# Kernel optimization log

Measured on AMD Instinct MI355X. Metric: run time of the kernel, lower is better.

The kernel has to match this reference:

```python
import jax, jax.numpy as jnp
import numpy as np

N, E, D, ED, H = 50000, 640000, 128, 64, 128
EPS = 1e-5


def _bn(x, gamma, beta):
    # BatchNorm1d in training mode: batch stats over rows, biased variance
    mean = jnp.mean(x, axis=0)
    var = jnp.mean(jnp.square(x - mean), axis=0)
    return (x - mean) * jax.lax.rsqrt(var + EPS) * gamma + beta


def setup_inputs() -> dict:
    key = jax.random.key(0)
    ks = jax.random.split(key, 12)

    def lin(k, fan_in, fan_out):
        return jax.random.normal(k, (fan_in, fan_out), jnp.float32) / np.sqrt(fan_in)

    return {
        "h": jax.random.normal(ks[0], (N, D), jnp.float32),
        "edge_attr": jax.random.normal(ks[1], (E, ED), jnp.float32),
        # msg MLP: Linear(2D+ED->H), BN(H), ReLU, Linear(H->H)
        "W1": lin(ks[2], 2 * D + ED, H), "b1": jnp.zeros((H,), jnp.float32),
        "g1": jnp.ones((H,), jnp.float32), "be1": jnp.zeros((H,), jnp.float32),
        "W2": lin(ks[3], H, H), "b2": jnp.zeros((H,), jnp.float32),
        # upd MLP: Linear(D+H->H), BN(H), ReLU, Linear(H->D)
        "W3": lin(ks[4], D + H, H), "b3": jnp.zeros((H,), jnp.float32),
        "g2": jnp.ones((H,), jnp.float32), "be2": jnp.zeros((H,), jnp.float32),
        "W4": lin(ks[5], H, D), "b4": jnp.zeros((D,), jnp.float32),
        # residual LayerNorm
        "ln_g": jnp.ones((D,), jnp.float32), "ln_b": jnp.zeros((D,), jnp.float32),
        "edge_index": jax.random.randint(ks[6], (2, E), 0, N, jnp.int32),
        "num_nodes": N,
    }


def reference(h, edge_attr, W1, b1, g1, be1, W2, b2, W3, b3, g2, be2, W4, b4,
              ln_g, ln_b, edge_index, num_nodes):
    src, dst = edge_index[0], edge_index[1]
    # messages: MLP_msg(h_src || h_dst || e)  -> [E, H]
    msg_in = jnp.concatenate([h[src], h[dst], edge_attr], axis=-1)  # [E, 2D+ED]
    x = _bn(msg_in @ W1 + b1, g1, be1)
    messages = jax.nn.relu(x) @ W2 + b2
    # scatter-sum aggregate into dst nodes -> [N, H]
    agg = jax.ops.segment_sum(messages, dst, num_segments=num_nodes)
    # update: MLP_upd(h || agg) -> [N, D]
    u = jnp.concatenate([h, agg], axis=-1)
    y = _bn(u @ W3 + b3, g2, be2)
    h_new = jax.nn.relu(y) @ W4 + b4
    # residual + LayerNorm
    z = h + h_new
    mu = jnp.mean(z, axis=-1, keepdims=True)
    var = jnp.mean(jnp.square(z - mu), axis=-1, keepdims=True)
    return (z - mu) * jax.lax.rsqrt(var + EPS) * ln_g + ln_b
```

## Files before the change

### kernel.cpp

```cpp
#include <hip/hip_runtime.h>
#include <hip/hip_bf16.h>

#define EPS 1e-5f
#define DIMH 128
#define K1 320
#define K3 256

typedef __attribute__((ext_vector_type(8))) short bf16x8;
typedef __attribute__((ext_vector_type(4))) short bf16x4;
typedef __attribute__((ext_vector_type(4))) float f32x4;

#define MFMA(a, b, c) __builtin_amdgcn_mfma_f32_16x16x32_bf16(a, b, c, 0, 0, 0)

static __device__ __forceinline__ unsigned short f2bf(float f) {
    union { float f; unsigned u; } v; v.f = f;
    unsigned r = v.u + 0x7FFF + ((v.u >> 16) & 1);
    return (unsigned short)(r >> 16);
}
static __device__ __forceinline__ float bf2f(unsigned short u) {
    union { unsigned u; float f; } v; v.u = ((unsigned)u) << 16;
    return v.f;
}

__global__ void k_prep(const float* __restrict__ W1, const float* __restrict__ W2,
                       const float* __restrict__ W3, const float* __restrict__ W4,
                       unsigned short* __restrict__ W1t, unsigned short* __restrict__ W2t,
                       unsigned short* __restrict__ W3t, unsigned short* __restrict__ W4t) {
    int t = blockIdx.x * 256 + threadIdx.x;
    if (t < K1 * 128) { int k = t / 128, n = t % 128; W1t[n * K1 + k] = f2bf(W1[t]); }
    if (t < 128 * 128) { int k = t / 128, n = t % 128; W2t[n * 128 + k] = f2bf(W2[t]); }
    if (t < K3 * 128) { int k = t / 128, n = t % 128; W3t[n * K3 + k] = f2bf(W3[t]); }
    if (t < 128 * 128) { int k = t / 128, n = t % 128; W4t[n * 128 + k] = f2bf(W4[t]); }
}

__global__ void k_bn(const float* __restrict__ stats, const float* __restrict__ g,
                     const float* __restrict__ be, float* __restrict__ st, float cnt) {
    int c = threadIdx.x;
    float mean = stats[c] / cnt;
    float var = stats[128 + c] / cnt - mean * mean;
    float s = g[c] * rsqrtf(var + EPS);
    st[c] = s;
    st[128 + c] = be[c] - mean * s;
}

__global__ __launch_bounds__(256, 2) void k_msg1(
    const float* __restrict__ h, const float* __restrict__ ea,
    const int* __restrict__ src, const int* __restrict__ dst,
    const unsigned short* __restrict__ W1t, const float* __restrict__ b1,
    unsigned short* __restrict__ xout, float* __restrict__ stats) {
    const int LDA = K1 + 8;
    __shared__ unsigned short A[64 * (K1 + 8)];
    int tid = threadIdx.x, lane = tid & 63, w = tid >> 6;
    long e0 = (long)blockIdx.x * 64;

    bf16x8 bfr[10][2];
    {
        int n = (w << 5) + (lane & 15), kb = (lane >> 4) << 3;
#pragma unroll
        for (int nt = 0; nt < 2; ++nt) {
            const unsigned short* p = W1t + (size_t)(n + nt * 16) * K1 + kb;
#pragma unroll
            for (int ks = 0; ks < 10; ++ks) bfr[ks][nt] = *(const bf16x8*)(p + ks * 32);
        }
    }
    {
        int c16 = tid & 15, r2 = tid >> 4;
#pragma unroll
        for (int rr = 0; rr < 4; ++rr) {
            int row = rr * 16 + r2;
            long e = e0 + row;
            const float* hs = h + (size_t)src[e] * DIMH;
            const float* hd = h + (size_t)dst[e] * DIMH;
            const float* ep = ea + (size_t)e * 64;
#pragma unroll
            for (int i = 0; i < 5; ++i) {
                int col = (c16 + (i << 4)) << 2;
                float4 v;
                if (col < 128) v = *(const float4*)(hs + col);
                else if (col < 256) v = *(const float4*)(hd + col - 128);
                else v = *(const float4*)(ep + col - 256);
                union { bf16x4 v4; unsigned short s[4]; } u;
                u.s[0] = f2bf(v.x); u.s[1] = f2bf(v.y); u.s[2] = f2bf(v.z); u.s[3] = f2bf(v.w);
                *(bf16x4*)&A[row * LDA + col] = u.v4;
            }
        }
    }
    __syncthreads();

    f32x4 acc[4][2] = {};
#pragma unroll
    for (int rg = 0; rg < 4; ++rg) {
        int ab = (rg * 16 + (lane & 15)) * LDA + ((lane >> 4) << 3);
#pragma unroll
        for (int ks = 0; ks < 10; ++ks) {
            bf16x8 af = *(const bf16x8*)&A[ab + ks * 32];
            acc[rg][0] = MFMA(af, bfr[ks][0], acc[rg][0]);
            acc[rg][1] = MFMA(af, bfr[ks][1], acc[rg][1]);
        }
    }
    int c0 = (w << 5) + (lane & 15);
    float bias0 = b1[c0], bias1 = b1[c0 + 16];
    float ss[2] = {0.f, 0.f}, sq[2] = {0.f, 0.f};
#pragma unroll
    for (int rg = 0; rg < 4; ++rg)
#pragma unroll
        for (int r = 0; r < 4; ++r) {
            long row = e0 + rg * 16 + ((lane >> 4) << 2) + r;
            float v0 = acc[rg][0][r] + bias0;
            float v1 = acc[rg][1][r] + bias1;
            ss[0] += v0; sq[0] += v0 * v0;
            ss[1] += v1; sq[1] += v1 * v1;
            xout[(size_t)row * DIMH + c0] = f2bf(v0);
            xout[(size_t)row * DIMH + c0 + 16] = f2bf(v1);
        }
#pragma unroll
    for (int nt = 0; nt < 2; ++nt) {
        ss[nt] += __shfl_xor(ss[nt], 16); ss[nt] += __shfl_xor(ss[nt], 32);
        sq[nt] += __shfl_xor(sq[nt], 16); sq[nt] += __shfl_xor(sq[nt], 32);
    }
    if (lane < 16) {
        atomicAdd(&stats[c0], ss[0]);        atomicAdd(&stats[c0 + 16], ss[1]);
        atomicAdd(&stats[128 + c0], sq[0]);  atomicAdd(&stats[128 + c0 + 16], sq[1]);
    }
}

__global__ __launch_bounds__(256, 2) void k_msg2(
    const unsigned short* __restrict__ x, const int* __restrict__ dst,
    const unsigned short* __restrict__ W2t, const float* __restrict__ b2,
    const float* __restrict__ st, float* __restrict__ agg) {
    const int LDA = 136;
    __shared__ unsigned short A[64 * 136];
    __shared__ float sS[128], sT[128];
    __shared__ int dstv[64];
    int tid = threadIdx.x, lane = tid & 63, w = tid >> 6;
    long e0 = (long)blockIdx.x * 64;
    if (tid < 128) { sS[tid] = st[tid]; sT[tid] = st[128 + tid]; }
    if (tid < 64) dstv[tid] = dst[e0 + tid];

    bf16x8 bfr[4][2];
    {
        int n = (w << 5) + (lane & 15), kb = (lane >> 4) << 3;
#pragma unroll
        for (int nt = 0; nt < 2; ++nt) {
            const unsigned short* p = W2t + (size_t)(n + nt * 16) * 128 + kb;
#pragma unroll
            for (int ks = 0; ks < 4; ++ks) bfr[ks][nt] = *(const bf16x8*)(p + ks * 32);
        }
    }
    __syncthreads();
    {
        int c16 = tid & 15, r2 = tid >> 4;
#pragma unroll
        for (int rr = 0; rr < 4; ++rr) {
            int row = rr * 16 + r2;
            bf16x8 v = *(const bf16x8*)(x + (size_t)(e0 + row) * DIMH + c16 * 8);
            union { bf16x8 v8; unsigned short s[8]; } u;
#pragma unroll
            for (int j = 0; j < 8; ++j) {
                int c = c16 * 8 + j;
                float f = bf2f((unsigned short)v[j]) * sS[c] + sT[c];
                u.s[j] = f2bf(fmaxf(f, 0.f));
            }
            *(bf16x8*)&A[row * LDA + c16 * 8] = u.v8;
        }
    }
    __syncthreads();

    f32x4 acc[4][2] = {};
#pragma unroll
    for (int rg = 0; rg < 4; ++rg) {
        int ab = (rg * 16 + (lane & 15)) * LDA + ((lane >> 4) << 3);
#pragma unroll
        for (int ks = 0; ks < 4; ++ks) {
            bf16x8 af = *(const bf16x8*)&A[ab + ks * 32];
            acc[rg][0] = MFMA(af, bfr[ks][0], acc[rg][0]);
            acc[rg][1] = MFMA(af, bfr[ks][1], acc[rg][1]);
        }
    }
    int c0 = (w << 5) + (lane & 15);
    float bias0 = b2[c0], bias1 = b2[c0 + 16];
#pragma unroll
    for (int rg = 0; rg < 4; ++rg)
#pragma unroll
        for (int r = 0; r < 4; ++r) {
            int row = rg * 16 + ((lane >> 4) << 2) + r;
            float* ap = agg + (size_t)dstv[row] * DIMH;
            atomicAdd(ap + c0, acc[rg][0][r] + bias0);
            atomicAdd(ap + c0 + 16, acc[rg][1][r] + bias1);
        }
}

__global__ __launch_bounds__(256, 2) void k_upd1(
    const float* __restrict__ h, const float* __restrict__ agg,
    const unsigned short* __restrict__ W3t, const float* __restrict__ b3,
    unsigned short* __restrict__ ypre, float* __restrict__ stats, int NN) {
    const int LDA = K3 + 8;
    __shared__ unsigned short A[64 * (K3 + 8)];
    int tid = threadIdx.x, lane = tid & 63, w = tid >> 6;
    int n0 = blockIdx.x * 64;

    bf16x8 bfr[8][2];
    {
        int n = (w << 5) + (lane & 15), kb = (lane >> 4) << 3;
#pragma unroll
        for (int nt = 0; nt < 2; ++nt) {
            const unsigned short* p = W3t + (size_t)(n + nt * 16) * K3 + kb;
#pragma unroll
            for (int ks = 0; ks < 8; ++ks) bfr[ks][nt] = *(const bf16x8*)(p + ks * 32);
        }
    }
    {
        int c16 = tid & 15, r2 = tid >> 4;
#pragma unroll
        for (int rr = 0; rr < 4; ++rr) {
            int row = rr * 16 + r2;
            int node = n0 + row;
#pragma unroll
            for (int i = 0; i < 4; ++i) {
                int col = (c16 + (i << 4)) << 2;
                float4 v = make_float4(0.f, 0.f, 0.f, 0.f);
                if (node < NN)
                    v = (col < 128) ? *(const float4*)(h + (size_t)node * DIMH + col)
                                    : *(const float4*)(agg + (size_t)node * DIMH + col - 128);
                union { bf16x4 v4; unsigned short s[4]; } u;
                u.s[0] = f2bf(v.x); u.s[1] = f2bf(v.y); u.s[2] = f2bf(v.z); u.s[3] = f2bf(v.w);
                *(bf16x4*)&A[row * LDA + col] = u.v4;
            }
        }
    }
    __syncthreads();

    f32x4 acc[4][2] = {};
#pragma unroll
    for (int rg = 0; rg < 4; ++rg) {
        int ab = (rg * 16 + (lane & 15)) * LDA + ((lane >> 4) << 3);
#pragma unroll
        for (int ks = 0; ks < 8; ++ks) {
            bf16x8 af = *(const bf16x8*)&A[ab + ks * 32];
            acc[rg][0] = MFMA(af, bfr[ks][0], acc[rg][0]);
            acc[rg][1] = MFMA(af, bfr[ks][1], acc[rg][1]);
        }
    }
    int c0 = (w << 5) + (lane & 15);
    float bias0 = b3[c0], bias1 = b3[c0 + 16];
    float ss[2] = {0.f, 0.f}, sq[2] = {0.f, 0.f};
#pragma unroll
    for (int rg = 0; rg < 4; ++rg)
#pragma unroll
        for (int r = 0; r < 4; ++r) {
            int node = n0 + rg * 16 + ((lane >> 4) << 2) + r;
            if (node < NN) {
                float v0 = acc[rg][0][r] + bias0;
                float v1 = acc[rg][1][r] + bias1;
                ss[0] += v0; sq[0] += v0 * v0;
                ss[1] += v1; sq[1] += v1 * v1;
                ypre[(size_t)node * DIMH + c0] = f2bf(v0);
                ypre[(size_t)node * DIMH + c0 + 16] = f2bf(v1);
            }
        }
#pragma unroll
    for (int nt = 0; nt < 2; ++nt) {
        ss[nt] += __shfl_xor(ss[nt], 16); ss[nt] += __shfl_xor(ss[nt], 32);
        sq[nt] += __shfl_xor(sq[nt], 16); sq[nt] += __shfl_xor(sq[nt], 32);
    }
    if (lane < 16) {
        atomicAdd(&stats[c0], ss[0]);        atomicAdd(&stats[c0 + 16], ss[1]);
        atomicAdd(&stats[128 + c0], sq[0]);  atomicAdd(&stats[128 + c0 + 16], sq[1]);
    }
}

__global__ __launch_bounds__(256, 2) void k_upd2(
    const unsigned short* __restrict__ ypre, const unsigned short* __restrict__ W4t,
    const float* __restrict__ b4, const float* __restrict__ st,
    const float* __restrict__ h, const float* __restrict__ lng,
    const float* __restrict__ lnb, float* __restrict__ out, int NN) {
    const int LDA = 136;
    __shared__ unsigned short A[64 * 136];
    __shared__ float sS[128], sT[128];
    __shared__ float rsum[64], rsq[64];
    int tid = threadIdx.x, lane = tid & 63, w = tid >> 6;
    int n0 = blockIdx.x * 64;
    if (tid < 128) { sS[tid] = st[tid]; sT[tid] = st[128 + tid]; }
    if (tid < 64) { rsum[tid] = 0.f; rsq[tid] = 0.f; }

    bf16x8 bfr[4][2];
    {
        int n = (w << 5) + (lane & 15), kb = (lane >> 4) << 3;
#pragma unroll
        for (int nt = 0; nt < 2; ++nt) {
            const unsigned short* p = W4t + (size_t)(n + nt * 16) * 128 + kb;
#pragma unroll
            for (int ks = 0; ks < 4; ++ks) bfr[ks][nt] = *(const bf16x8*)(p + ks * 32);
        }
    }
    __syncthreads();
    {
        int c16 = tid & 15, r2 = tid >> 4;
#pragma unroll
        for (int rr = 0; rr < 4; ++rr) {
            int row = rr * 16 + r2;
            int node = n0 + row;
            union { bf16x8 v8; unsigned short s[8]; } u;
            if (node < NN) {
                bf16x8 v = *(const bf16x8*)(ypre + (size_t)node * DIMH + c16 * 8);
#pragma unroll
                for (int j = 0; j < 8; ++j) {
                    int c = c16 * 8 + j;
                    float f = bf2f((unsigned short)v[j]) * sS[c] + sT[c];
                    u.s[j] = f2bf(fmaxf(f, 0.f));
                }
            } else {
#pragma unroll
                for (int j = 0; j < 8; ++j) u.s[j] = 0;
            }
            *(bf16x8*)&A[row * LDA + c16 * 8] = u.v8;
        }
    }
    __syncthreads();

    f32x4 acc[4][2] = {};
#pragma unroll
    for (int rg = 0; rg < 4; ++rg) {
        int ab = (rg * 16 + (lane & 15)) * LDA + ((lane >> 4) << 3);
#pragma unroll
        for (int ks = 0; ks < 4; ++ks) {
            bf16x8 af = *(const bf16x8*)&A[ab + ks * 32];
            acc[rg][0] = MFMA(af, bfr[ks][0], acc[rg][0]);
            acc[rg][1] = MFMA(af, bfr[ks][1], acc[rg][1]);
        }
    }
    int c0 = (w << 5) + (lane & 15);
    float bias0 = b4[c0], bias1 = b4[c0 + 16];
    float z[4][2][4];
#pragma unroll
    for (int rg = 0; rg < 4; ++rg)
#pragma unroll
        for (int r = 0; r < 4; ++r) {
            int node = n0 + rg * 16 + ((lane >> 4) << 2) + r;
            float h0 = 0.f, h1 = 0.f;
            if (node < NN) {
                h0 = h[(size_t)node * DIMH + c0];
                h1 = h[(size_t)node * DIMH + c0 + 16];
            }
            z[rg][0][r] = acc[rg][0][r] + bias0 + h0;
            z[rg][1][r] = acc[rg][1][r] + bias1 + h1;
        }
#pragma unroll
    for (int rg = 0; rg < 4; ++rg)
#pragma unroll
        for (int r = 0; r < 4; ++r) {
            float ps = z[rg][0][r] + z[rg][1][r];
            float pq = z[rg][0][r] * z[rg][0][r] + z[rg][1][r] * z[rg][1][r];
#pragma unroll
            for (int m = 1; m < 16; m <<= 1) { ps += __shfl_xor(ps, m); pq += __shfl_xor(pq, m); }
            if ((lane & 15) == 0) {
                int row = rg * 16 + ((lane >> 4) << 2) + r;
                atomicAdd(&rsum[row], ps);
                atomicAdd(&rsq[row], pq);
            }
        }
    __syncthreads();
#pragma unroll
    for (int rg = 0; rg < 4; ++rg)
#pragma unroll
        for (int r = 0; r < 4; ++r) {
            int row = rg * 16 + ((lane >> 4) << 2) + r;
            int node = n0 + row;
            if (node < NN) {
                float mean = rsum[row] * (1.f / 128.f);
                float var = rsq[row] * (1.f / 128.f) - mean * mean;
                float rs = rsqrtf(var + EPS);
                float g0 = lng[c0], g1 = lng[c0 + 16];
                float be0 = lnb[c0], be1 = lnb[c0 + 16];
                out[(size_t)node * DIMH + c0] = (z[rg][0][r] - mean) * rs * g0 + be0;
                out[(size_t)node * DIMH + c0 + 16] = (z[rg][1][r] - mean) * rs * g1 + be1;
            }
        }
}

extern "C" void kernel_launch(void* const* d_in, const int* in_sizes, int n_in,
                              void* d_out, int out_size, void* d_ws, size_t ws_size,
                              hipStream_t stream) {
    const float* h   = (const float*)d_in[0];
    const float* ea  = (const float*)d_in[1];
    const float* W1  = (const float*)d_in[2];
    const float* b1  = (const float*)d_in[3];
    const float* g1  = (const float*)d_in[4];
    const float* be1 = (const float*)d_in[5];
    const float* W2  = (const float*)d_in[6];
    const float* b2  = (const float*)d_in[7];
    const float* W3  = (const float*)d_in[8];
    const float* b3  = (const float*)d_in[9];
    const float* g2  = (const float*)d_in[10];
    const float* be2 = (const float*)d_in[11];
    const float* W4  = (const float*)d_in[12];
    const float* b4  = (const float*)d_in[13];
    const float* lng = (const float*)d_in[14];
    const float* lnb = (const float*)d_in[15];
    const int* eidx  = (const int*)d_in[16];
    int NN = in_sizes[0] / DIMH;
    int E  = in_sizes[16] / 2;
    const int* src = eidx;
    const int* dst = eidx + E;

    char* ws = (char*)d_ws;
    unsigned short* W1t = (unsigned short*)(ws + 0);
    unsigned short* W2t = (unsigned short*)(ws + 81920);
    unsigned short* W3t = (unsigned short*)(ws + 114688);
    unsigned short* W4t = (unsigned short*)(ws + 180224);
    float* stats1 = (float*)(ws + 212992);
    float* st1    = (float*)(ws + 214016);
    float* stats2 = (float*)(ws + 215040);
    float* st2    = (float*)(ws + 216064);
    unsigned short* x = (unsigned short*)(ws + 217088);
    float* agg = (float*)(ws + 217088 + 163840000ULL);
    unsigned short* ypre = (unsigned short*)(ws + 217088 + 163840000ULL + 25600000ULL);

    hipMemsetAsync(stats1, 0, 1024, stream);
    hipMemsetAsync(stats2, 0, 1024, stream);
    hipMemsetAsync(agg, 0, (size_t)NN * DIMH * sizeof(float), stream);

    k_prep<<<(K1 * 128 + 255) / 256, 256, 0, stream>>>(W1, W2, W3, W4, W1t, W2t, W3t, W4t);
    k_msg1<<<E / 64, 256, 0, stream>>>(h, ea, src, dst, W1t, b1, x, stats1);
    k_bn<<<1, 128, 0, stream>>>(stats1, g1, be1, st1, (float)E);
    k_msg2<<<E / 64, 256, 0, stream>>>(x, dst, W2t, b2, st1, agg);
    int nb = (NN + 63) / 64;
    k_upd1<<<nb, 256, 0, stream>>>(h, agg, W3t, b3, ypre, stats2, NN);
    k_bn<<<1, 128, 0, stream>>>(stats2, g2, be2, st2, (float)NN);
    k_upd2<<<nb, 256, 0, stream>>>(ypre, W4t, b4, st2, h, lng, lnb, (float*)d_out, NN);
}
```

Baseline: 826.6 us.

## Fold W2 into W3 and replace atomic scatter with CSR gather aggregation

```diff
diff --git a/kernel.cpp b/kernel.cpp
--- a/kernel.cpp
+++ b/kernel.cpp
@@ -17,20 +17,47 @@
     unsigned r = v.u + 0x7FFF + ((v.u >> 16) & 1);
     return (unsigned short)(r >> 16);
 }
-static __device__ __forceinline__ float bf2f(unsigned short u) {
-    union { unsigned u; float f; } v; v.u = ((unsigned)u) << 16;
-    return v.f;
-}
-
-__global__ void k_prep(const float* __restrict__ W1, const float* __restrict__ W2,
-                       const float* __restrict__ W3, const float* __restrict__ W4,
-                       unsigned short* __restrict__ W1t, unsigned short* __restrict__ W2t,
-                       unsigned short* __restrict__ W3t, unsigned short* __restrict__ W4t) {
+
+__global__ void k_prep_w(const float* __restrict__ W1, const float* __restrict__ W3,
+                         const float* __restrict__ W4,
+                         unsigned short* __restrict__ W1t, unsigned short* __restrict__ W3c,
+                         unsigned short* __restrict__ W4t) {
     int t = blockIdx.x * 256 + threadIdx.x;
     if (t < K1 * 128) { int k = t / 128, n = t % 128; W1t[n * K1 + k] = f2bf(W1[t]); }
-    if (t < 128 * 128) { int k = t / 128, n = t % 128; W2t[n * 128 + k] = f2bf(W2[t]); }
-    if (t < K3 * 128) { int k = t / 128, n = t % 128; W3t[n * K3 + k] = f2bf(W3[t]); }
-    if (t < 128 * 128) { int k = t / 128, n = t % 128; W4t[n * 128 + k] = f2bf(W4[t]); }
+    if (t < 128 * 128) {
+        int k = t / 128, n = t % 128;
+        W4t[n * 128 + k] = f2bf(W4[t]);
+        W3c[n * K3 + k] = f2bf(W3[t]);
+    }
+}
+
+__global__ void k_hb(const float* __restrict__ h, unsigned short* __restrict__ hb, int total8) {
+    int t = blockIdx.x * 256 + threadIdx.x;
+    if (t < total8) {
+        float4 a = *(const float4*)(h + (size_t)t * 8);
+        float4 b = *(const float4*)(h + (size_t)t * 8 + 4);
+        union { bf16x8 v; unsigned short s[8]; } u;
+        u.s[0] = f2bf(a.x); u.s[1] = f2bf(a.y); u.s[2] = f2bf(a.z); u.s[3] = f2bf(a.w);
+        u.s[4] = f2bf(b.x); u.s[5] = f2bf(b.y); u.s[6] = f2bf(b.z); u.s[7] = f2bf(b.w);
+        *(bf16x8*)(hb + (size_t)t * 8) = u.v;
+    }
+}
+
+__global__ void k_w23(const float* __restrict__ W2, const float* __restrict__ W3,
+                      unsigned short* __restrict__ W3c) {
+    int t = blockIdx.x * 256 + threadIdx.x;
+    int j = t & 127, i = t >> 7;
+    float s = 0.f;
+    for (int k = 0; k < 128; ++k) s += W2[i * 128 + k] * W3[(128 + k) * 128 + j];
+    W3c[j * K3 + 128 + i] = f2bf(s);
+}
+
+__global__ void k_cvec(const float* __restrict__ b2, const float* __restrict__ W3,
+                       float* __restrict__ cvec) {
+    int j = threadIdx.x;
+    float s = 0.f;
+    for (int k = 0; k < 128; ++k) s += b2[k] * W3[(128 + k) * 128 + j];
+    cvec[j] = s;
 }
 
 __global__ void k_bn(const float* __restrict__ stats, const float* __restrict__ g,
@@ -43,13 +70,48 @@
     st[128 + c] = be[c] - mean * s;
 }
 
-__global__ __launch_bounds__(256, 2) void k_msg1(
-    const float* __restrict__ h, const float* __restrict__ ea,
+__global__ void k_deg(const int* __restrict__ dst, int* __restrict__ deg, int E) {
+    int e = blockIdx.x * 256 + threadIdx.x;
+    if (e < E) atomicAdd(&deg[dst[e]], 1);
+}
+
+__global__ void k_scan(const int* __restrict__ deg, int* __restrict__ offs,
+                       int* __restrict__ cursor, int NN) {
+    __shared__ int ps[1024];
+    int t = threadIdx.x;
+    int chunk = (NN + 1023) >> 10;
+    int c0 = t * chunk;
+    int s = 0;
+    for (int i = 0; i < chunk; ++i) { int id = c0 + i; if (id < NN) s += deg[id]; }
+    ps[t] = s; __syncthreads();
+    for (int off = 1; off < 1024; off <<= 1) {
+        int v = (t >= off) ? ps[t - off] : 0;
+        __syncthreads();
+        ps[t] += v;
+        __syncthreads();
+    }
+    int run = t ? ps[t - 1] : 0;
+    for (int i = 0; i < chunk; ++i) {
+        int id = c0 + i;
+        if (id < NN) { cursor[id] = run; run += deg[id]; offs[id] = run; }
+    }
+}
+
+__global__ void k_scatter(const int* __restrict__ dst, int* __restrict__ cursor,
+                          int* __restrict__ elist, int E) {
+    int e = blockIdx.x * 256 + threadIdx.x;
+    if (e < E) {
+        int pos = atomicAdd(&cursor[dst[e]], 1);
+        elist[pos] = e;
+    }
+}
+
+__global__ __launch_bounds__(256, 4) void k_msg1(
+    const unsigned short* __restrict__ hb, const float* __restrict__ ea,
     const int* __restrict__ src, const int* __restrict__ dst,
     const unsigned short* __restrict__ W1t, const float* __restrict__ b1,
     unsigned short* __restrict__ xout, float* __restrict__ stats) {
-    const int LDA = K1 + 8;
-    __shared__ unsigned short A[64 * (K1 + 8)];
+    __shared__ unsigned short A[64 * K1];
     int tid = threadIdx.x, lane = tid & 63, w = tid >> 6;
     long e0 = (long)blockIdx.x * 64;
 
@@ -69,20 +131,16 @@
         for (int rr = 0; rr < 4; ++rr) {
             int row = rr * 16 + r2;
             long e = e0 + row;
-            const float* hs = h + (size_t)src[e] * DIMH;
-            const float* hd = h + (size_t)dst[e] * DIMH;
-            const float* ep = ea + (size_t)e * 64;
-#pragma unroll
-            for (int i = 0; i < 5; ++i) {
-                int col = (c16 + (i << 4)) << 2;
-                float4 v;
-                if (col < 128) v = *(const float4*)(hs + col);
-                else if (col < 256) v = *(const float4*)(hd + col - 128);
-                else v = *(const float4*)(ep + col - 256);
-                union { bf16x4 v4; unsigned short s[4]; } u;
-                u.s[0] = f2bf(v.x); u.s[1] = f2bf(v.y); u.s[2] = f2bf(v.z); u.s[3] = f2bf(v.w);
-                *(bf16x4*)&A[row * LDA + col] = u.v4;
-            }
+            int s = src[e], d = dst[e];
+            bf16x8 vs = *(const bf16x8*)(hb + (size_t)s * DIMH + c16 * 8);
+            bf16x8 vd = *(const bf16x8*)(hb + (size_t)d * DIMH + c16 * 8);
+            float4 ve = *(const float4*)(ea + (size_t)e * 64 + c16 * 4);
+            int base = row * K1, sw = (row & 7) << 3;
+            *(bf16x8*)&A[(base + c16 * 8) ^ sw] = vs;
+            *(bf16x8*)&A[(base + 128 + c16 * 8) ^ sw] = vd;
+            union { bf16x4 v4; unsigned short s4[4]; } u;
+            u.s4[0] = f2bf(ve.x); u.s4[1] = f2bf(ve.y); u.s4[2] = f2bf(ve.z); u.s4[3] = f2bf(ve.w);
+            *(bf16x4*)&A[(base + 256 + c16 * 4) ^ sw] = u.v4;
         }
     }
     __syncthreads();
@@ -90,10 +148,11 @@
     f32x4 acc[4][2] = {};
 #pragma unroll
     for (int rg = 0; rg < 4; ++rg) {
-        int ab = (rg * 16 + (lane & 15)) * LDA + ((lane >> 4) << 3);
+        int arow = rg * 16 + (lane & 15);
+        int base = arow * K1, sw = (arow & 7) << 3, kb = (lane >> 4) << 3;
 #pragma unroll
         for (int ks = 0; ks < 10; ++ks) {
-            bf16x8 af = *(const bf16x8*)&A[ab + ks * 32];
+            bf16x8 af = *(const bf16x8*)&A[(base + ks * 32 + kb) ^ sw];
             acc[rg][0] = MFMA(af, bfr[ks][0], acc[rg][0]);
             acc[rg][1] = MFMA(af, bfr[ks][1], acc[rg][1]);
         }
@@ -124,78 +183,44 @@
     }
 }
 
-__global__ __launch_bounds__(256, 2) void k_msg2(
-    const unsigned short* __restrict__ x, const int* __restrict__ dst,
-    const unsigned short* __restrict__ W2t, const float* __restrict__ b2,
-    const float* __restrict__ st, float* __restrict__ agg) {
-    const int LDA = 136;
-    __shared__ unsigned short A[64 * 136];
-    __shared__ float sS[128], sT[128];
-    __shared__ int dstv[64];
-    int tid = threadIdx.x, lane = tid & 63, w = tid >> 6;
-    long e0 = (long)blockIdx.x * 64;
-    if (tid < 128) { sS[tid] = st[tid]; sT[tid] = st[128 + tid]; }
-    if (tid < 64) dstv[tid] = dst[e0 + tid];
-
-    bf16x8 bfr[4][2];
-    {
-        int n = (w << 5) + (lane & 15), kb = (lane >> 4) << 3;
-#pragma unroll
-        for (int nt = 0; nt < 2; ++nt) {
-            const unsigned short* p = W2t + (size_t)(n + nt * 16) * 128 + kb;
-#pragma unroll
-            for (int ks = 0; ks < 4; ++ks) bfr[ks][nt] = *(const bf16x8*)(p + ks * 32);
-        }
-    }
-    __syncthreads();
-    {
-        int c16 = tid & 15, r2 = tid >> 4;
-#pragma unroll
-        for (int rr = 0; rr < 4; ++rr) {
-            int row = rr * 16 + r2;
-            bf16x8 v = *(const bf16x8*)(x + (size_t)(e0 + row) * DIMH + c16 * 8);
-            union { bf16x8 v8; unsigned short s[8]; } u;
-#pragma unroll
-            for (int j = 0; j < 8; ++j) {
-                int c = c16 * 8 + j;
-                float f = bf2f((unsigned short)v[j]) * sS[c] + sT[c];
-                u.s[j] = f2bf(fmaxf(f, 0.f));
-            }
-            *(bf16x8*)&A[row * LDA + c16 * 8] = u.v8;
-        }
-    }
-    __syncthreads();
-
-    f32x4 acc[4][2] = {};
-#pragma unroll
-    for (int rg = 0; rg < 4; ++rg) {
-        int ab = (rg * 16 + (lane & 15)) * LDA + ((lane >> 4) << 3);
-#pragma unroll
-        for (int ks = 0; ks < 4; ++ks) {
-            bf16x8 af = *(const bf16x8*)&A[ab + ks * 32];
-            acc[rg][0] = MFMA(af, bfr[ks][0], acc[rg][0]);
-            acc[rg][1] = MFMA(af, bfr[ks][1], acc[rg][1]);
-        }
-    }
-    int c0 = (w << 5) + (lane & 15);
-    float bias0 = b2[c0], bias1 = b2[c0 + 16];
-#pragma unroll
-    for (int rg = 0; rg < 4; ++rg)
-#pragma unroll
-        for (int r = 0; r < 4; ++r) {
-            int row = rg * 16 + ((lane >> 4) << 2) + r;
-            float* ap = agg + (size_t)dstv[row] * DIMH;
-            atomicAdd(ap + c0, acc[rg][0][r] + bias0);
-            atomicAdd(ap + c0 + 16, acc[rg][1][r] + bias1);
-        }
-}
-
-__global__ __launch_bounds__(256, 2) void k_upd1(
-    const float* __restrict__ h, const float* __restrict__ agg,
-    const unsigned short* __restrict__ W3t, const float* __restrict__ b3,
+__global__ __launch_bounds__(256, 8) void k_agg(
+    const unsigned short* __restrict__ x, const float* __restrict__ st,
+    const int* __restrict__ offs, const int* __restrict__ deg,
+    const int* __restrict__ elist, float* __restrict__ R, int NN) {
+    int lane = threadIdx.x & 63, w = threadIdx.x >> 6;
+    int n = blockIdx.x * 4 + w;
+    if (n >= NN) return;
+    int c = lane * 2;
+    float s0 = st[c], s1 = st[c + 1], t0 = st[128 + c], t1 = st[128 + c + 1];
+    int end = offs[n], start = end - deg[n];
+    float a0 = 0.f, a1 = 0.f;
+    int i = start;
+    for (; i + 1 < end; i += 2) {
+        int e0 = elist[i], e1 = elist[i + 1];
+        unsigned v0 = *(const unsigned*)(x + (size_t)e0 * DIMH + c);
+        unsigned v1 = *(const unsigned*)(x + (size_t)e1 * DIMH + c);
+        float f;
+        f = __uint_as_float(v0 << 16) * s0 + t0;         a0 += fmaxf(f, 0.f);
+        f = __uint_as_float(v0 & 0xffff0000u) * s1 + t1; a1 += fmaxf(f, 0.f);
+        f = __uint_as_float(v1 << 16) * s0 + t0;         a0 += fmaxf(f, 0.f);
+        f = __uint_as_float(v1 & 0xffff0000u) * s1 + t1; a1 += fmaxf(f, 0.f);
+    }
+    if (i < end) {
+        int e0 = elist[i];
+        unsigned v0 = *(const unsigned*)(x + (size_t)e0 * DIMH + c);
+        float f;
+        f = __uint_as_float(v0 << 16) * s0 + t0;         a0 += fmaxf(f, 0.f);
+        f = __uint_as_float(v0 & 0xffff0000u) * s1 + t1; a1 += fmaxf(f, 0.f);
+    }
+    *(float2*)(R + (size_t)n * DIMH + c) = make_float2(a0, a1);
+}
+
+__global__ __launch_bounds__(256, 4) void k_upd1(
+    const unsigned short* __restrict__ hb, const float* __restrict__ R,
+    const unsigned short* __restrict__ W3c, const float* __restrict__ b3,
+    const int* __restrict__ deg, const float* __restrict__ cvec,
     unsigned short* __restrict__ ypre, float* __restrict__ stats, int NN) {
-    const int LDA = K3 + 8;
-    __shared__ unsigned short A[64 * (K3 + 8)];
+    __shared__ unsigned short A[64 * K3];
     int tid = threadIdx.x, lane = tid & 63, w = tid >> 6;
     int n0 = blockIdx.x * 64;
 
@@ -204,7 +229,7 @@
         int n = (w << 5) + (lane & 15), kb = (lane >> 4) << 3;
 #pragma unroll
         for (int nt = 0; nt < 2; ++nt) {
-            const unsigned short* p = W3t + (size_t)(n + nt * 16) * K3 + kb;
+            const unsigned short* p = W3c + (size_t)(n + nt * 16) * K3 + kb;
 #pragma unroll
             for (int ks = 0; ks < 8; ++ks) bfr[ks][nt] = *(const bf16x8*)(p + ks * 32);
         }
@@ -215,17 +240,21 @@
         for (int rr = 0; rr < 4; ++rr) {
             int row = rr * 16 + r2;
             int node = n0 + row;
-#pragma unroll
-            for (int i = 0; i < 4; ++i) {
-                int col = (c16 + (i << 4)) << 2;
-                float4 v = make_float4(0.f, 0.f, 0.f, 0.f);
-                if (node < NN)
-                    v = (col < 128) ? *(const float4*)(h + (size_t)node * DIMH + col)
-                                    : *(const float4*)(agg + (size_t)node * DIMH + col - 128);
-                union { bf16x4 v4; unsigned short s[4]; } u;
-                u.s[0] = f2bf(v.x); u.s[1] = f2bf(v.y); u.s[2] = f2bf(v.z); u.s[3] = f2bf(v.w);
-                *(bf16x4*)&A[row * LDA + col] = u.v4;
-            }
+            bf16x8 vh = {};
+            union { bf16x8 v8; unsigned short s8[8]; } ur;
+            if (node < NN) {
+                vh = *(const bf16x8*)(hb + (size_t)node * DIMH + c16 * 8);
+                float4 r0 = *(const float4*)(R + (size_t)node * DIMH + c16 * 8);
+                float4 r1 = *(const float4*)(R + (size_t)node * DIMH + c16 * 8 + 4);
+                ur.s8[0] = f2bf(r0.x); ur.s8[1] = f2bf(r0.y); ur.s8[2] = f2bf(r0.z); ur.s8[3] = f2bf(r0.w);
+                ur.s8[4] = f2bf(r1.x); ur.s8[5] = f2bf(r1.y); ur.s8[6] = f2bf(r1.z); ur.s8[7] = f2bf(r1.w);
+            } else {
+#pragma unroll
+                for (int j = 0; j < 8; ++j) ur.s8[j] = 0;
+            }
+            int base = row * K3, sw = (row & 7) << 3;
+            *(bf16x8*)&A[(base + c16 * 8) ^ sw] = vh;
+            *(bf16x8*)&A[(base + 128 + c16 * 8) ^ sw] = ur.v8;
         }
     }
     __syncthreads();
@@ -233,16 +262,18 @@
     f32x4 acc[4][2] = {};
 #pragma unroll
     for (int rg = 0; rg < 4; ++rg) {
-        int ab = (rg * 16 + (lane & 15)) * LDA + ((lane >> 4) << 3);
+        int arow = rg * 16 + (lane & 15);
+        int base = arow * K3, sw = (arow & 7) << 3, kb = (lane >> 4) << 3;
 #pragma unroll
         for (int ks = 0; ks < 8; ++ks) {
-            bf16x8 af = *(const bf16x8*)&A[ab + ks * 32];
+            bf16x8 af = *(const bf16x8*)&A[(base + ks * 32 + kb) ^ sw];
             acc[rg][0] = MFMA(af, bfr[ks][0], acc[rg][0]);
             acc[rg][1] = MFMA(af, bfr[ks][1], acc[rg][1]);
         }
     }
     int c0 = (w << 5) + (lane & 15);
     float bias0 = b3[c0], bias1 = b3[c0 + 16];
+    float cv0 = cvec[c0], cv1 = cvec[c0 + 16];
     float ss[2] = {0.f, 0.f}, sq[2] = {0.f, 0.f};
 #pragma unroll
     for (int rg = 0; rg < 4; ++rg)
@@ -250,8 +281,9 @@
         for (int r = 0; r < 4; ++r) {
             int node = n0 + rg * 16 + ((lane >> 4) << 2) + r;
             if (node < NN) {
-                float v0 = acc[rg][0][r] + bias0;
-                float v1 = acc[rg][1][r] + bias1;
+                float dg = (float)deg[node];
+                float v0 = acc[rg][0][r] + bias0 + dg * cv0;
+                float v1 = acc[rg][1][r] + bias1 + dg * cv1;
                 ss[0] += v0; sq[0] += v0 * v0;
                 ss[1] += v1; sq[1] += v1 * v1;
                 ypre[(size_t)node * DIMH + c0] = f2bf(v0);
@@ -306,7 +338,8 @@
 #pragma unroll
                 for (int j = 0; j < 8; ++j) {
                     int c = c16 * 8 + j;
-                    float f = bf2f((unsigned short)v[j]) * sS[c] + sT[c];
+                    union { unsigned uu; float f; } cvt; cvt.uu = ((unsigned)(unsigned short)v[j]) << 16;
+                    float f = cvt.f * sS[c] + sT[c];
                     u.s[j] = f2bf(fmaxf(f, 0.f));
                 }
             } else {
@@ -404,28 +437,42 @@
     const int* dst = eidx + E;
 
     char* ws = (char*)d_ws;
-    unsigned short* W1t = (unsigned short*)(ws + 0);
-    unsigned short* W2t = (unsigned short*)(ws + 81920);
-    unsigned short* W3t = (unsigned short*)(ws + 114688);
-    unsigned short* W4t = (unsigned short*)(ws + 180224);
-    float* stats1 = (float*)(ws + 212992);
-    float* st1    = (float*)(ws + 214016);
-    float* stats2 = (float*)(ws + 215040);
-    float* st2    = (float*)(ws + 216064);
-    unsigned short* x = (unsigned short*)(ws + 217088);
-    float* agg = (float*)(ws + 217088 + 163840000ULL);
-    unsigned short* ypre = (unsigned short*)(ws + 217088 + 163840000ULL + 25600000ULL);
+    size_t o = 0;
+    unsigned short* W1t = (unsigned short*)(ws + o); o += 81920;
+    unsigned short* W3c = (unsigned short*)(ws + o); o += 65536;
+    unsigned short* W4t = (unsigned short*)(ws + o); o += 32768;
+    float* cvec   = (float*)(ws + o); o += 512;
+    float* stats1 = (float*)(ws + o); o += 1024;
+    float* st1    = (float*)(ws + o); o += 1024;
+    float* stats2 = (float*)(ws + o); o += 1024;
+    float* st2    = (float*)(ws + o); o += 1024;
+    int* deg    = (int*)(ws + o); o += 200192;
+    int* offs   = (int*)(ws + o); o += 200192;
+    int* cursor = (int*)(ws + o); o += 200192;
+    int* elist  = (int*)(ws + o); o += (size_t)E * 4;
+    unsigned short* hb = (unsigned short*)(ws + o); o += (size_t)NN * DIMH * 2;
+    float* R = (float*)(ws + o); o += (size_t)NN * DIMH * 4;
+    unsigned short* x = (unsigned short*)(ws + o);
+    unsigned short* ypre = x;
 
     hipMemsetAsync(stats1, 0, 1024, stream);
     hipMemsetAsync(stats2, 0, 1024, stream);
-    hipMemsetAsync(agg, 0, (size_t)NN * DIMH * sizeof(float), stream);
-
-    k_prep<<<(K1 * 128 + 255) / 256, 256, 0, stream>>>(W1, W2, W3, W4, W1t, W2t, W3t, W4t);
-    k_msg1<<<E / 64, 256, 0, stream>>>(h, ea, src, dst, W1t, b1, x, stats1);
+    hipMemsetAsync(deg, 0, (size_t)NN * 4, stream);
+
+    k_prep_w<<<(K1 * 128 + 255) / 256, 256, 0, stream>>>(W1, W3, W4, W1t, W3c, W4t);
+    k_hb<<<(NN * DIMH / 8 + 255) / 256, 256, 0, stream>>>(h, hb, NN * DIMH / 8);
+    k_w23<<<64, 256, 0, stream>>>(W2, W3, W3c);
+    k_cvec<<<1, 128, 0, stream>>>(b2, W3, cvec);
+    k_deg<<<(E + 255) / 256, 256, 0, stream>>>(dst, deg, E);
+    k_scan<<<1, 1024, 0, stream>>>(deg, offs, cursor, NN);
+    k_scatter<<<(E + 255) / 256, 256, 0, stream>>>(dst, cursor, elist, E);
+
+    k_msg1<<<E / 64, 256, 0, stream>>>(hb, ea, src, dst, W1t, b1, x, stats1);
     k_bn<<<1, 128, 0, stream>>>(stats1, g1, be1, st1, (float)E);
-    k_msg2<<<E / 64, 256, 0, stream>>>(x, dst, W2t, b2, st1, agg);
+    k_agg<<<(NN + 3) / 4, 256, 0, stream>>>(x, st1, offs, deg, elist, R, NN);
+
     int nb = (NN + 63) / 64;
-    k_upd1<<<nb, 256, 0, stream>>>(h, agg, W3t, b3, ypre, stats2, NN);
+    k_upd1<<<nb, 256, 0, stream>>>(hb, R, W3c, b3, deg, cvec, ypre, stats2, NN);
     k_bn<<<1, 128, 0, stream>>>(stats2, g2, be2, st2, (float)NN);
     k_upd2<<<nb, 256, 0, stream>>>(ypre, W4t, b4, st2, h, lng, lnb, (float*)d_out, NN);
 }
```

Result: no change. 832.9 us (+0.8%).
